# Kernel optimization log

Hardware: AMD Instinct MI355X
Metric: run time of the kernel (lower is better)

Reference implementation:

```python
import jax, jax.numpy as jnp
import numpy as np

B, N, F_IN = 8, 2048, 256
H, D = 4, 64  # num_heads, out_per_head (H*D == F_IN for residual)
ALPHA = 0.2   # leakyrelu slope


def setup_inputs() -> dict:
    key = jax.random.key(0)
    k1, k2, k3 = jax.random.split(key, 3)
    h = jax.random.normal(k1, (B, N, F_IN), dtype=jnp.float32)
    adj = jax.random.uniform(k2, (B, N, N), dtype=jnp.float32)
    # stacked per-head Linear weights (no bias): [H, F_in, D]
    W = jax.random.normal(k3, (H, F_IN, D), dtype=jnp.float32) * (1.0 / np.sqrt(F_IN))
    return {"h": h, "adj": adj, "W": W}


def reference(h, adj, W):
    # NOTE: in the original module, adj goes through drop_edge but is never
    # used in the attention computation, so it has no effect on the output.
    # P: per-head projections [B, H, N, D]
    P = jnp.einsum("bnf,hfd->bhnd", h, W)
    # scores: leakyrelu(P P^T) [B, H, N, N]
    scores = jnp.einsum("bhnd,bhmd->bhnm", P, P)
    scores = jnp.where(scores > 0, scores, ALPHA * scores)
    attn = jax.nn.softmax(scores, axis=-1)
    out = jnp.einsum("bhnm,bhmd->bhnd", attn, P)
    # concat heads along feature dim: [B, N, H*D]
    out = out.transpose(0, 2, 1, 3).reshape(h.shape[0], h.shape[1], -1)
    return out + h
```

## Files before the change

kernel.cpp:

```cpp
#include <hip/hip_runtime.h>
#include <cstdint>

#define B_    8
#define N_    2048
#define FIN_  256
#define H_    4
#define D_    64
#define NEG_SLOPE 0.2f
#define LOG2E 1.44269504f

typedef __bf16    bf16x8 __attribute__((ext_vector_type(8)));
typedef _Float16  f16x8  __attribute__((ext_vector_type(8)));
typedef __fp16    fp16x2 __attribute__((ext_vector_type(2)));
typedef uint16_t  u16x8  __attribute__((ext_vector_type(8)));
typedef float     fx4    __attribute__((ext_vector_type(4)));

static __device__ __forceinline__ float bf2f(uint16_t u) {
    union { uint32_t u; float f; } c; c.u = ((uint32_t)u) << 16; return c.f;
}
static __device__ __forceinline__ uint16_t f2bf(float f) {
    union { float f; uint32_t u; } c; c.f = f;
    return (uint16_t)((c.u + 0x7fffu + ((c.u >> 16) & 1u)) >> 16);
}
static __device__ __forceinline__ uint16_t f2h(float f) {
    const _Float16 h = (_Float16)f;
    return __builtin_bit_cast(uint16_t, h);
}
static __device__ __forceinline__ bf16x8 ldbf8(const uint16_t* p) {
    return *(const bf16x8*)p;
}
static __device__ __forceinline__ f16x8 ldf8(const uint16_t* p) {
    return *(const f16x8*)p;
}
static __device__ __forceinline__ bf16x8 asbf(u16x8 v) {
    union { u16x8 u; bf16x8 b; } c; c.u = v; return c.b;
}
static __device__ __forceinline__ void split8(const float* p, bf16x8& hi, bf16x8& lo) {
    const float4 x0 = *(const float4*)p;
    const float4 x1 = *(const float4*)(p + 4);
    const float f[8] = {x0.x, x0.y, x0.z, x0.w, x1.x, x1.y, x1.z, x1.w};
    u16x8 h, l;
    #pragma unroll
    for (int j = 0; j < 8; ++j) {
        const uint16_t hb = f2bf(f[j]);
        h[j] = hb;
        l[j] = f2bf(f[j] - bf2f(hb));
    }
    hi = asbf(h); lo = asbf(l);
}
static __device__ __forceinline__ uint32_t pkh2(float a, float b) {
    const fp16x2 h = __builtin_amdgcn_cvt_pkrtz(a, b);
    return __builtin_bit_cast(uint32_t, h);
}

__global__ void prep_kernel(const float* __restrict__ W,
                            uint16_t* __restrict__ Wt_hi,
                            uint16_t* __restrict__ Wt_lo) {
    const int h  = blockIdx.x >> 4;
    const int d4 = blockIdx.x & 15;
    const int f  = threadIdx.x;
    const float4 w = *(const float4*)(W + (((size_t)h * FIN_ + f) * D_ + d4 * 4));
    const float vv[4] = {w.x, w.y, w.z, w.w};
    #pragma unroll
    for (int j = 0; j < 4; ++j) {
        const int d = d4 * 4 + j;
        const uint16_t hb = f2bf(vv[j]);
        Wt_hi[((size_t)h * D_ + d) * FIN_ + f] = hb;
        Wt_lo[((size_t)h * D_ + d) * FIN_ + f] = f2bf(vv[j] - bf2f(hb));
    }
}

__global__ __launch_bounds__(256, 2) void proj_kernel(
    const float*    __restrict__ hin,
    const uint16_t* __restrict__ Wt_hi,
    const uint16_t* __restrict__ Wt_lo,
    uint16_t* __restrict__ P_f16,
    uint16_t* __restrict__ Pt_f16)
{
    __shared__ __align__(16) uint16_t plds[4][16][72];

    const int lane = threadIdx.x & 63, wave = threadIdx.x >> 6;
    const int quad = lane >> 4, l15 = lane & 15;

    const int b  = blockIdx.y;
    const int h0 = blockIdx.z * 2;
    const int n0 = blockIdx.x * 64 + wave * 16;

    const float* arow = hin + ((size_t)b * N_ + n0 + l15) * FIN_ + quad * 8;

    fx4 acc[2][4];
    #pragma unroll
    for (int hh = 0; hh < 2; ++hh)
        #pragma unroll
        for (int t = 0; t < 4; ++t) acc[hh][t] = (fx4)(0.0f);

    #pragma unroll
    for (int k0 = 0; k0 < FIN_; k0 += 32) {
        bf16x8 ahi, alo;
        split8(arow + k0, ahi, alo);
        #pragma unroll
        for (int hh = 0; hh < 2; ++hh) {
            const uint16_t* whi = Wt_hi + (size_t)(h0 + hh) * D_ * FIN_;
            const uint16_t* wlo = Wt_lo + (size_t)(h0 + hh) * D_ * FIN_;
            #pragma unroll
            for (int t = 0; t < 4; ++t) {
                const size_t off = (size_t)(t * 16 + l15) * FIN_ + k0 + quad * 8;
                const bf16x8 bhi = ldbf8(whi + off);
                const bf16x8 blo = ldbf8(wlo + off);
                acc[hh][t] = __builtin_amdgcn_mfma_f32_16x16x32_bf16(ahi, bhi, acc[hh][t], 0, 0, 0);
                acc[hh][t] = __builtin_amdgcn_mfma_f32_16x16x32_bf16(alo, bhi, acc[hh][t], 0, 0, 0);
                acc[hh][t] = __builtin_amdgcn_mfma_f32_16x16x32_bf16(ahi, blo, acc[hh][t], 0, 0, 0);
            }
        }
    }

    #pragma unroll
    for (int hh = 0; hh < 2; ++hh) {
        const int bh = b * H_ + h0 + hh;
        #pragma unroll
        for (int t = 0; t < 4; ++t)
            #pragma unroll
            for (int r = 0; r < 4; ++r)
                plds[wave][quad * 4 + r][t * 16 + l15] = f2h(acc[hh][t][r]);

        {
            const uint16_t* base = &plds[wave][l15][0];
            const int4 r0 = *(const int4*)(base + quad * 8);
            const int4 r1 = *(const int4*)(base + quad * 8 + 32);
            uint16_t* pg = P_f16 + ((size_t)bh * N_ + n0 + l15) * D_;
            *(int4*)(pg + quad * 8)      = r0;
            *(int4*)(pg + quad * 8 + 32) = r1;
        }
        {
            uint32_t u[8];
            #pragma unroll
            for (int j = 0; j < 8; ++j) {
                const uint16_t e0 = plds[wave][2 * j][lane];
                const uint16_t e1 = plds[wave][2 * j + 1][lane];
                u[j] = (uint32_t)e0 | ((uint32_t)e1 << 16);
            }
            uint16_t* pt = Pt_f16 + ((size_t)bh * D_ + lane) * N_ + n0;
            int4 s0, s1;
            s0.x = u[0]; s0.y = u[1]; s0.z = u[2]; s0.w = u[3];
            s1.x = u[4]; s1.y = u[5]; s1.z = u[6]; s1.w = u[7];
            *(int4*)pt       = s0;
            *(int4*)(pt + 8) = s1;
        }
    }
}

__global__ __launch_bounds__(256, 4) void attn_kernel(
    const uint16_t* __restrict__ P_f16,
    const uint16_t* __restrict__ Pt_f16,
    const float*    __restrict__ hin,
    float*          __restrict__ out)
{
    __shared__ __align__(16) uint16_t sK[64 * 64];
    __shared__ __align__(16) uint16_t sV[64 * 64];
    __shared__ __align__(16) uint16_t plds[4][16][72];

    const int tid  = threadIdx.x;
    const int lane = tid & 63, wave = tid >> 6;
    const int quad = lane >> 4, l15 = lane & 15;

    const int bh = blockIdx.y, b = bh >> 2, hd = bh & 3;
    const int n0 = blockIdx.x * 64 + wave * 16;

    const uint16_t* Pf = P_f16  + (size_t)bh * N_ * D_;
    const uint16_t* Pt = Pt_f16 + (size_t)bh * D_ * N_;

    f16x8 qf[2];
    {
        const uint16_t* qrow = Pf + (size_t)(n0 + l15) * D_ + quad * 8;
        qf[0] = ldf8(qrow); qf[1] = ldf8(qrow + 32);
        const _Float16 c = (_Float16)LOG2E;
        #pragma unroll
        for (int j = 0; j < 8; ++j) { qf[0][j] *= c; qf[1][j] *= c; }
    }

    const int i0 = tid, i1 = tid + 256;
    const int r0s = i0 >> 3, c0s = i0 & 7;
    const int r1s = i1 >> 3, c1s = i1 & 7;
    const uint16_t* gK0 = Pf + (size_t)r0s * D_ + (c0s ^ (r0s & 7)) * 8;
    const uint16_t* gK1 = Pf + (size_t)r1s * D_ + (c1s ^ (r1s & 7)) * 8;
    const uint16_t* gV0 = Pt + (size_t)r0s * N_ + (c0s ^ (r0s & 7)) * 8;
    const uint16_t* gV1 = Pt + (size_t)r1s * N_ + (c1s ^ (r1s & 7)) * 8;

    int4 rK0 = *(const int4*)gK0, rK1 = *(const int4*)gK1;
    int4 rV0 = *(const int4*)gV0, rV1 = *(const int4*)gV1;

    float m_i = -1e30f, l_i = 0.0f;
    fx4 oacc[4];
    #pragma unroll
    for (int dt = 0; dt < 4; ++dt) oacc[dt] = (fx4)(0.0f);

    const int cc = quad ^ (l15 & 7);

    for (int it = 0; it < N_ / 64; ++it) {
        __syncthreads();
        ((int4*)sK)[i0] = rK0; ((int4*)sK)[i1] = rK1;
        ((int4*)sV)[i0] = rV0; ((int4*)sV)[i1] = rV1;
        const int knx = (it < N_ / 64 - 1) ? (it + 1) * 64 : 0;
        rK0 = *(const int4*)(gK0 + (size_t)knx * D_);
        rK1 = *(const int4*)(gK1 + (size_t)knx * D_);
        rV0 = *(const int4*)(gV0 + knx);
        rV1 = *(const int4*)(gV1 + knx);
        __syncthreads();

        fx4 s[4];
        #pragma unroll
        for (int t = 0; t < 4; ++t) s[t] = (fx4)(0.0f);
        #pragma unroll
        for (int t = 0; t < 4; ++t) {
            const uint16_t* kb = sK + (t * 16 + l15) * 64;
            const f16x8 k0 = ldf8(kb + cc * 8);
            const f16x8 k1 = ldf8(kb + (cc ^ 4) * 8);
            s[t] = __builtin_amdgcn_mfma_f32_16x16x32_f16(k0, qf[0], s[t], 0, 0, 0);
            s[t] = __builtin_amdgcn_mfma_f32_16x16x32_f16(k1, qf[1], s[t], 0, 0, 0);
        }

        float pm[16];
        #pragma unroll
        for (int t = 0; t < 4; ++t)
            #pragma unroll
            for (int r = 0; r < 4; ++r) {
                const float v = s[t][r];
                pm[t * 4 + r] = fmaxf(v, NEG_SLOPE * v);
            }
        float mx = pm[0];
        #pragma unroll
        for (int j = 1; j < 16; ++j) mx = fmaxf(mx, pm[j]);
        mx = fmaxf(mx, __shfl_xor(mx, 16));
        mx = fmaxf(mx, __shfl_xor(mx, 32));
        const float mnew  = fmaxf(m_i, mx);
        const float alpha = __builtin_amdgcn_exp2f(m_i - mnew);
        float rs = 0.0f;
        #pragma unroll
        for (int j = 0; j < 16; ++j) {
            const float e = __builtin_amdgcn_exp2f(pm[j] - mnew);
            pm[j] = e; rs += e;
        }
        rs += __shfl_xor(rs, 16);
        rs += __shfl_xor(rs, 32);
        l_i = l_i * alpha + rs;
        m_i = mnew;
        #pragma unroll
        for (int dt = 0; dt < 4; ++dt)
            #pragma unroll
            for (int r = 0; r < 4; ++r) oacc[dt][r] *= alpha;

        #pragma unroll
        for (int t = 0; t < 4; ++t) {
            const uint32_t w0 = pkh2(pm[t * 4 + 0], pm[t * 4 + 1]);
            const uint32_t w1 = pkh2(pm[t * 4 + 2], pm[t * 4 + 3]);
            uint2* dst = (uint2*)&plds[wave][l15][t * 16 + quad * 4];
            *dst = make_uint2(w0, w1);
        }
        const f16x8 a0 = ldf8(&plds[wave][l15][quad * 8]);
        const f16x8 a1 = ldf8(&plds[wave][l15][32 + quad * 8]);

        #pragma unroll
        for (int dt = 0; dt < 4; ++dt) {
            const uint16_t* vb = sV + (dt * 16 + l15) * 64;
            const f16x8 v0 = ldf8(vb + cc * 8);
            const f16x8 v1 = ldf8(vb + (cc ^ 4) * 8);
            oacc[dt] = __builtin_amdgcn_mfma_f32_16x16x32_f16(v0, a0, oacc[dt], 0, 0, 0);
            oacc[dt] = __builtin_amdgcn_mfma_f32_16x16x32_f16(v1, a1, oacc[dt], 0, 0, 0);
        }
    }

    const float inv = 1.0f / l_i;
    const size_t rowbase = ((size_t)b * N_ + n0 + l15) * FIN_ + hd * D_;
    #pragma unroll
    for (int dt = 0; dt < 4; ++dt)
        #pragma unroll
        for (int r = 0; r < 4; ++r) {
            const size_t idx = rowbase + dt * 16 + quad * 4 + r;
            out[idx] = oacc[dt][r] * inv + hin[idx];
        }
}

extern "C" void kernel_launch(void* const* d_in, const int* in_sizes, int n_in,
                              void* d_out, int out_size, void* d_ws, size_t ws_size,
                              hipStream_t stream) {
    const float* hin = (const float*)d_in[0];
    const float* W   = (const float*)d_in[2];
    float* out = (float*)d_out;

    uint16_t* Wt_hi = (uint16_t*)d_ws;
    uint16_t* Wt_lo = Wt_hi + (size_t)H_ * D_ * FIN_;
    uint16_t* P_f16 = Wt_lo + (size_t)H_ * D_ * FIN_;
    uint16_t* Pt_f16= P_f16 + (size_t)B_ * H_ * N_ * D_;

    hipLaunchKernelGGL(prep_kernel, dim3(H_ * 16),         dim3(FIN_), 0, stream, W, Wt_hi, Wt_lo);
    hipLaunchKernelGGL(proj_kernel, dim3(N_/64, B_, H_/2), dim3(256),  0, stream,
                       hin, Wt_hi, Wt_lo, P_f16, Pt_f16);
    hipLaunchKernelGGL(attn_kernel, dim3(N_/64, B_*H_),    dim3(256),  0, stream,
                       P_f16, Pt_f16, hin, out);
}
```

Baseline: 278.3 us.

## Drop online softmax max, use self-score offset, bf16 PV, double-buffered 32-row tiles

The projection now uses a single fp16 MFMA per tile instead of a three-pass bf16 hi/lo split. The attention kernel removes the running-max online softmax and subtracts a fixed per-row offset instead: the query's own squared norm, which is the self-score. Row sums are computed with an MFMA against a ones vector, and P and V are stored as bf16, with P truncated rather than rounded. Each wave now handles 32 query rows, and K/V tiles are double-buffered in LDS with one barrier per iteration. In exchange, precision drops, and the fixed offset risks overflow or underflow if some score is far above the self-score.

Measured after the change: 253.0 us. 9.1% less time.

```diff
diff --git a/kernel.cpp b/kernel.cpp
--- a/kernel.cpp
+++ b/kernel.cpp
@@ -11,7 +11,6 @@
 
 typedef __bf16    bf16x8 __attribute__((ext_vector_type(8)));
 typedef _Float16  f16x8  __attribute__((ext_vector_type(8)));
-typedef __fp16    fp16x2 __attribute__((ext_vector_type(2)));
 typedef uint16_t  u16x8  __attribute__((ext_vector_type(8)));
 typedef float     fx4    __attribute__((ext_vector_type(4)));
 
@@ -32,30 +31,23 @@
 static __device__ __forceinline__ f16x8 ldf8(const uint16_t* p) {
     return *(const f16x8*)p;
 }
-static __device__ __forceinline__ bf16x8 asbf(u16x8 v) {
-    union { u16x8 u; bf16x8 b; } c; c.u = v; return c.b;
-}
-static __device__ __forceinline__ void split8(const float* p, bf16x8& hi, bf16x8& lo) {
+static __device__ __forceinline__ uint32_t pkbf_trunc(float lo, float hi) {
+    const uint32_t ul = __builtin_bit_cast(uint32_t, lo);
+    const uint32_t uh = __builtin_bit_cast(uint32_t, hi);
+    return (ul >> 16) | (uh & 0xFFFF0000u);
+}
+static __device__ __forceinline__ f16x8 cvt8(const float* p) {
     const float4 x0 = *(const float4*)p;
     const float4 x1 = *(const float4*)(p + 4);
     const float f[8] = {x0.x, x0.y, x0.z, x0.w, x1.x, x1.y, x1.z, x1.w};
-    u16x8 h, l;
-    #pragma unroll
-    for (int j = 0; j < 8; ++j) {
-        const uint16_t hb = f2bf(f[j]);
-        h[j] = hb;
-        l[j] = f2bf(f[j] - bf2f(hb));
-    }
-    hi = asbf(h); lo = asbf(l);
-}
-static __device__ __forceinline__ uint32_t pkh2(float a, float b) {
-    const fp16x2 h = __builtin_amdgcn_cvt_pkrtz(a, b);
-    return __builtin_bit_cast(uint32_t, h);
+    f16x8 r;
+    #pragma unroll
+    for (int j = 0; j < 8; ++j) r[j] = (_Float16)f[j];
+    return r;
 }
 
 __global__ void prep_kernel(const float* __restrict__ W,
-                            uint16_t* __restrict__ Wt_hi,
-                            uint16_t* __restrict__ Wt_lo) {
+                            uint16_t* __restrict__ Wt_f16) {
     const int h  = blockIdx.x >> 4;
     const int d4 = blockIdx.x & 15;
     const int f  = threadIdx.x;
@@ -64,18 +56,15 @@
     #pragma unroll
     for (int j = 0; j < 4; ++j) {
         const int d = d4 * 4 + j;
-        const uint16_t hb = f2bf(vv[j]);
-        Wt_hi[((size_t)h * D_ + d) * FIN_ + f] = hb;
-        Wt_lo[((size_t)h * D_ + d) * FIN_ + f] = f2bf(vv[j] - bf2f(hb));
+        Wt_f16[((size_t)h * D_ + d) * FIN_ + f] = f2h(vv[j]);
     }
 }
 
 __global__ __launch_bounds__(256, 2) void proj_kernel(
     const float*    __restrict__ hin,
-    const uint16_t* __restrict__ Wt_hi,
-    const uint16_t* __restrict__ Wt_lo,
+    const uint16_t* __restrict__ Wt_f16,
     uint16_t* __restrict__ P_f16,
-    uint16_t* __restrict__ Pt_f16)
+    uint16_t* __restrict__ Pt_bf16)
 {
     __shared__ __align__(16) uint16_t plds[4][16][72];
 
@@ -96,20 +85,14 @@
 
     #pragma unroll
     for (int k0 = 0; k0 < FIN_; k0 += 32) {
-        bf16x8 ahi, alo;
-        split8(arow + k0, ahi, alo);
+        const f16x8 a = cvt8(arow + k0);
         #pragma unroll
         for (int hh = 0; hh < 2; ++hh) {
-            const uint16_t* whi = Wt_hi + (size_t)(h0 + hh) * D_ * FIN_;
-            const uint16_t* wlo = Wt_lo + (size_t)(h0 + hh) * D_ * FIN_;
+            const uint16_t* wb = Wt_f16 + (size_t)(h0 + hh) * D_ * FIN_;
             #pragma unroll
             for (int t = 0; t < 4; ++t) {
-                const size_t off = (size_t)(t * 16 + l15) * FIN_ + k0 + quad * 8;
-                const bf16x8 bhi = ldbf8(whi + off);
-                const bf16x8 blo = ldbf8(wlo + off);
-                acc[hh][t] = __builtin_amdgcn_mfma_f32_16x16x32_bf16(ahi, bhi, acc[hh][t], 0, 0, 0);
-                acc[hh][t] = __builtin_amdgcn_mfma_f32_16x16x32_bf16(alo, bhi, acc[hh][t], 0, 0, 0);
-                acc[hh][t] = __builtin_amdgcn_mfma_f32_16x16x32_bf16(ahi, blo, acc[hh][t], 0, 0, 0);
+                const f16x8 bb = ldf8(wb + (size_t)(t * 16 + l15) * FIN_ + k0 + quad * 8);
+                acc[hh][t] = __builtin_amdgcn_mfma_f32_16x16x32_f16(a, bb, acc[hh][t], 0, 0, 0);
             }
         }
     }
@@ -122,7 +105,6 @@
             #pragma unroll
             for (int r = 0; r < 4; ++r)
                 plds[wave][quad * 4 + r][t * 16 + l15] = f2h(acc[hh][t][r]);
-
         {
             const uint16_t* base = &plds[wave][l15][0];
             const int4 r0 = *(const int4*)(base + quad * 8);
@@ -131,6 +113,11 @@
             *(int4*)(pg + quad * 8)      = r0;
             *(int4*)(pg + quad * 8 + 32) = r1;
         }
+        #pragma unroll
+        for (int t = 0; t < 4; ++t)
+            #pragma unroll
+            for (int r = 0; r < 4; ++r)
+                plds[wave][quad * 4 + r][t * 16 + l15] = f2bf(acc[hh][t][r]);
         {
             uint32_t u[8];
             #pragma unroll
@@ -139,7 +126,7 @@
                 const uint16_t e1 = plds[wave][2 * j + 1][lane];
                 u[j] = (uint32_t)e0 | ((uint32_t)e1 << 16);
             }
-            uint16_t* pt = Pt_f16 + ((size_t)bh * D_ + lane) * N_ + n0;
+            uint16_t* pt = Pt_bf16 + ((size_t)bh * D_ + lane) * N_ + n0;
             int4 s0, s1;
             s0.x = u[0]; s0.y = u[1]; s0.z = u[2]; s0.w = u[3];
             s1.x = u[4]; s1.y = u[5]; s1.z = u[6]; s1.w = u[7];
@@ -149,33 +136,56 @@
     }
 }
 
-__global__ __launch_bounds__(256, 4) void attn_kernel(
+__global__ __launch_bounds__(256, 2) void attn_kernel(
     const uint16_t* __restrict__ P_f16,
-    const uint16_t* __restrict__ Pt_f16,
+    const uint16_t* __restrict__ Pt_bf16,
     const float*    __restrict__ hin,
     float*          __restrict__ out)
 {
-    __shared__ __align__(16) uint16_t sK[64 * 64];
-    __shared__ __align__(16) uint16_t sV[64 * 64];
-    __shared__ __align__(16) uint16_t plds[4][16][72];
+    __shared__ __align__(16) uint16_t sK[2][64 * 64];
+    __shared__ __align__(16) uint16_t sV[2][64 * 64];
+    __shared__ __align__(16) uint16_t plds[4][32][72];
 
     const int tid  = threadIdx.x;
     const int lane = tid & 63, wave = tid >> 6;
     const int quad = lane >> 4, l15 = lane & 15;
 
     const int bh = blockIdx.y, b = bh >> 2, hd = bh & 3;
-    const int n0 = blockIdx.x * 64 + wave * 16;
-
-    const uint16_t* Pf = P_f16  + (size_t)bh * N_ * D_;
-    const uint16_t* Pt = Pt_f16 + (size_t)bh * D_ * N_;
-
-    f16x8 qf[2];
+    const int n0 = blockIdx.x * 128 + wave * 32;
+
+    const uint16_t* Pf = P_f16   + (size_t)bh * N_ * D_;
+    const uint16_t* Pt = Pt_bf16 + (size_t)bh * D_ * N_;
+
+    f16x8 qf[2][2];
+    #pragma unroll
+    for (int mt = 0; mt < 2; ++mt) {
+        const uint16_t* qrow = Pf + (size_t)(n0 + mt * 16 + l15) * D_ + quad * 8;
+        qf[mt][0] = ldf8(qrow); qf[mt][1] = ldf8(qrow + 32);
+        const _Float16 c = (_Float16)LOG2E;
+        #pragma unroll
+        for (int j = 0; j < 8; ++j) { qf[mt][0][j] *= c; qf[mt][1][j] *= c; }
+    }
+
+    float C[2];
+    #pragma unroll
+    for (int mt = 0; mt < 2; ++mt) {
+        float acc = 0.0f;
+        #pragma unroll
+        for (int j = 0; j < 8; ++j) {
+            const float a0 = (float)qf[mt][0][j], a1 = (float)qf[mt][1][j];
+            acc += a0 * a0 + a1 * a1;
+        }
+        acc += __shfl_xor(acc, 16);
+        acc += __shfl_xor(acc, 32);
+        C[mt] = acc * (1.0f / LOG2E);
+    }
+
+    bf16x8 ones;
     {
-        const uint16_t* qrow = Pf + (size_t)(n0 + l15) * D_ + quad * 8;
-        qf[0] = ldf8(qrow); qf[1] = ldf8(qrow + 32);
-        const _Float16 c = (_Float16)LOG2E;
-        #pragma unroll
-        for (int j = 0; j < 8; ++j) { qf[0][j] *= c; qf[1][j] *= c; }
+        u16x8 ov;
+        #pragma unroll
+        for (int j = 0; j < 8; ++j) ov[j] = 0x3F80;
+        ones = __builtin_bit_cast(bf16x8, ov);
     }
 
     const int i0 = tid, i1 = tid + 256;
@@ -186,98 +196,118 @@
     const uint16_t* gV0 = Pt + (size_t)r0s * N_ + (c0s ^ (r0s & 7)) * 8;
     const uint16_t* gV1 = Pt + (size_t)r1s * N_ + (c1s ^ (r1s & 7)) * 8;
 
-    int4 rK0 = *(const int4*)gK0, rK1 = *(const int4*)gK1;
-    int4 rV0 = *(const int4*)gV0, rV1 = *(const int4*)gV1;
-
-    float m_i = -1e30f, l_i = 0.0f;
-    fx4 oacc[4];
-    #pragma unroll
-    for (int dt = 0; dt < 4; ++dt) oacc[dt] = (fx4)(0.0f);
+    {
+        int4 a = *(const int4*)gK0, bb = *(const int4*)gK1;
+        int4 c = *(const int4*)gV0, d  = *(const int4*)gV1;
+        ((int4*)sK[0])[i0] = a;  ((int4*)sK[0])[i1] = bb;
+        ((int4*)sV[0])[i0] = c;  ((int4*)sV[0])[i1] = d;
+    }
+    int4 rK0 = *(const int4*)(gK0 + (size_t)64 * D_);
+    int4 rK1 = *(const int4*)(gK1 + (size_t)64 * D_);
+    int4 rV0 = *(const int4*)(gV0 + 64);
+    int4 rV1 = *(const int4*)(gV1 + 64);
+
+    fx4 oacc[2][4], lacc[2];
+    #pragma unroll
+    for (int mt = 0; mt < 2; ++mt) {
+        lacc[mt] = (fx4)(0.0f);
+        #pragma unroll
+        for (int dt = 0; dt < 4; ++dt) oacc[mt][dt] = (fx4)(0.0f);
+    }
 
     const int cc = quad ^ (l15 & 7);
 
+    __syncthreads();
     for (int it = 0; it < N_ / 64; ++it) {
-        __syncthreads();
-        ((int4*)sK)[i0] = rK0; ((int4*)sK)[i1] = rK1;
-        ((int4*)sV)[i0] = rV0; ((int4*)sV)[i1] = rV1;
-        const int knx = (it < N_ / 64 - 1) ? (it + 1) * 64 : 0;
-        rK0 = *(const int4*)(gK0 + (size_t)knx * D_);
-        rK1 = *(const int4*)(gK1 + (size_t)knx * D_);
-        rV0 = *(const int4*)(gV0 + knx);
-        rV1 = *(const int4*)(gV1 + knx);
-        __syncthreads();
-
-        fx4 s[4];
-        #pragma unroll
-        for (int t = 0; t < 4; ++t) s[t] = (fx4)(0.0f);
+        const int cur = it & 1;
+        if (it < N_ / 64 - 1) {
+            ((int4*)sK[cur ^ 1])[i0] = rK0; ((int4*)sK[cur ^ 1])[i1] = rK1;
+            ((int4*)sV[cur ^ 1])[i0] = rV0; ((int4*)sV[cur ^ 1])[i1] = rV1;
+        }
+        if (it < N_ / 64 - 2) {
+            const size_t ko = (size_t)(it + 2) * 64;
+            rK0 = *(const int4*)(gK0 + ko * D_);
+            rK1 = *(const int4*)(gK1 + ko * D_);
+            rV0 = *(const int4*)(gV0 + ko);
+            rV1 = *(const int4*)(gV1 + ko);
+        }
+
+        fx4 s[2][4];
+        #pragma unroll
+        for (int mt = 0; mt < 2; ++mt)
+            #pragma unroll
+            for (int t = 0; t < 4; ++t) s[mt][t] = (fx4)(0.0f);
         #pragma unroll
         for (int t = 0; t < 4; ++t) {
-            const uint16_t* kb = sK + (t * 16 + l15) * 64;
+            const uint16_t* kb = &sK[cur][(t * 16 + l15) * 64];
             const f16x8 k0 = ldf8(kb + cc * 8);
             const f16x8 k1 = ldf8(kb + (cc ^ 4) * 8);
-            s[t] = __builtin_amdgcn_mfma_f32_16x16x32_f16(k0, qf[0], s[t], 0, 0, 0);
-            s[t] = __builtin_amdgcn_mfma_f32_16x16x32_f16(k1, qf[1], s[t], 0, 0, 0);
-        }
-
-        float pm[16];
-        #pragma unroll
-        for (int t = 0; t < 4; ++t)
-            #pragma unroll
-            for (int r = 0; r < 4; ++r) {
-                const float v = s[t][r];
-                pm[t * 4 + r] = fmaxf(v, NEG_SLOPE * v);
-            }
-        float mx = pm[0];
-        #pragma unroll
-        for (int j = 1; j < 16; ++j) mx = fmaxf(mx, pm[j]);
-        mx = fmaxf(mx, __shfl_xor(mx, 16));
-        mx = fmaxf(mx, __shfl_xor(mx, 32));
-        const float mnew  = fmaxf(m_i, mx);
-        const float alpha = __builtin_amdgcn_exp2f(m_i - mnew);
-        float rs = 0.0f;
-        #pragma unroll
-        for (int j = 0; j < 16; ++j) {
-            const float e = __builtin_amdgcn_exp2f(pm[j] - mnew);
-            pm[j] = e; rs += e;
-        }
-        rs += __shfl_xor(rs, 16);
-        rs += __shfl_xor(rs, 32);
-        l_i = l_i * alpha + rs;
-        m_i = mnew;
-        #pragma unroll
-        for (int dt = 0; dt < 4; ++dt)
-            #pragma unroll
-            for (int r = 0; r < 4; ++r) oacc[dt][r] *= alpha;
-
-        #pragma unroll
-        for (int t = 0; t < 4; ++t) {
-            const uint32_t w0 = pkh2(pm[t * 4 + 0], pm[t * 4 + 1]);
-            const uint32_t w1 = pkh2(pm[t * 4 + 2], pm[t * 4 + 3]);
-            uint2* dst = (uint2*)&plds[wave][l15][t * 16 + quad * 4];
-            *dst = make_uint2(w0, w1);
-        }
-        const f16x8 a0 = ldf8(&plds[wave][l15][quad * 8]);
-        const f16x8 a1 = ldf8(&plds[wave][l15][32 + quad * 8]);
-
+            #pragma unroll
+            for (int mt = 0; mt < 2; ++mt) {
+                s[mt][t] = __builtin_amdgcn_mfma_f32_16x16x32_f16(k0, qf[mt][0], s[mt][t], 0, 0, 0);
+                s[mt][t] = __builtin_amdgcn_mfma_f32_16x16x32_f16(k1, qf[mt][1], s[mt][t], 0, 0, 0);
+            }
+        }
+
+        #pragma unroll
+        for (int mt = 0; mt < 2; ++mt) {
+            #pragma unroll
+            for (int t = 0; t < 4; ++t) {
+                float e[4];
+                #pragma unroll
+                for (int r = 0; r < 4; ++r) {
+                    const float v = s[mt][t][r];
+                    e[r] = __builtin_amdgcn_exp2f(fmaxf(v, NEG_SLOPE * v) - C[mt]);
+                }
+                const uint32_t w0 = pkbf_trunc(e[0], e[1]);
+                const uint32_t w1 = pkbf_trunc(e[2], e[3]);
+                *(uint2*)&plds[wave][mt * 16 + l15][t * 16 + quad * 4] = make_uint2(w0, w1);
+            }
+        }
+
+        bf16x8 a[2][2];
+        #pragma unroll
+        for (int mt = 0; mt < 2; ++mt) {
+            const uint16_t* pb = &plds[wave][mt * 16 + l15][0];
+            a[mt][0] = ldbf8(pb + quad * 8);
+            a[mt][1] = ldbf8(pb + quad * 8 + 32);
+        }
+
+        #pragma unroll
+        for (int mt = 0; mt < 2; ++mt) {
+            lacc[mt] = __builtin_amdgcn_mfma_f32_16x16x32_bf16(ones, a[mt][0], lacc[mt], 0, 0, 0);
+            lacc[mt] = __builtin_amdgcn_mfma_f32_16x16x32_bf16(ones, a[mt][1], lacc[mt], 0, 0, 0);
+        }
         #pragma unroll
         for (int dt = 0; dt < 4; ++dt) {
-            const uint16_t* vb = sV + (dt * 16 + l15) * 64;
-            const f16x8 v0 = ldf8(vb + cc * 8);
-            const f16x8 v1 = ldf8(vb + (cc ^ 4) * 8);
-            oacc[dt] = __builtin_amdgcn_mfma_f32_16x16x32_f16(v0, a0, oacc[dt], 0, 0, 0);
-            oacc[dt] = __builtin_amdgcn_mfma_f32_16x16x32_f16(v1, a1, oacc[dt], 0, 0, 0);
-        }
-    }
-
-    const float inv = 1.0f / l_i;
-    const size_t rowbase = ((size_t)b * N_ + n0 + l15) * FIN_ + hd * D_;
-    #pragma unroll
-    for (int dt = 0; dt < 4; ++dt)
-        #pragma unroll
-        for (int r = 0; r < 4; ++r) {
-            const size_t idx = rowbase + dt * 16 + quad * 4 + r;
-            out[idx] = oacc[dt][r] * inv + hin[idx];
-        }
+            const uint16_t* vb = &sV[cur][(dt * 16 + l15) * 64];
+            const bf16x8 v0 = ldbf8(vb + cc * 8);
+            const bf16x8 v1 = ldbf8(vb + (cc ^ 4) * 8);
+            #pragma unroll
+            for (int mt = 0; mt < 2; ++mt) {
+                oacc[mt][dt] = __builtin_amdgcn_mfma_f32_16x16x32_bf16(v0, a[mt][0], oacc[mt][dt], 0, 0, 0);
+                oacc[mt][dt] = __builtin_amdgcn_mfma_f32_16x16x32_bf16(v1, a[mt][1], oacc[mt][dt], 0, 0, 0);
+            }
+        }
+        __syncthreads();
+    }
+
+    #pragma unroll
+    for (int mt = 0; mt < 2; ++mt) {
+        const float inv = 1.0f / lacc[mt][0];
+        const size_t rowbase = ((size_t)b * N_ + n0 + mt * 16 + l15) * FIN_ + hd * D_;
+        #pragma unroll
+        for (int dt = 0; dt < 4; ++dt) {
+            const size_t idx = rowbase + dt * 16 + quad * 4;
+            const float4 hv = *(const float4*)&hin[idx];
+            float4 o;
+            o.x = oacc[mt][dt][0] * inv + hv.x;
+            o.y = oacc[mt][dt][1] * inv + hv.y;
+            o.z = oacc[mt][dt][2] * inv + hv.z;
+            o.w = oacc[mt][dt][3] * inv + hv.w;
+            *(float4*)&out[idx] = o;
+        }
+    }
 }
 
 extern "C" void kernel_launch(void* const* d_in, const int* in_sizes, int n_in,
@@ -287,14 +317,13 @@
     const float* W   = (const float*)d_in[2];
     float* out = (float*)d_out;
 
-    uint16_t* Wt_hi = (uint16_t*)d_ws;
-    uint16_t* Wt_lo = Wt_hi + (size_t)H_ * D_ * FIN_;
-    uint16_t* P_f16 = Wt_lo + (size_t)H_ * D_ * FIN_;
-    uint16_t* Pt_f16= P_f16 + (size_t)B_ * H_ * N_ * D_;
-
-    hipLaunchKernelGGL(prep_kernel, dim3(H_ * 16),         dim3(FIN_), 0, stream, W, Wt_hi, Wt_lo);
+    uint16_t* Wt_f16  = (uint16_t*)d_ws;
+    uint16_t* P_f16   = Wt_f16 + (size_t)H_ * D_ * FIN_;
+    uint16_t* Pt_bf16 = P_f16  + (size_t)B_ * H_ * N_ * D_;
+
+    hipLaunchKernelGGL(prep_kernel, dim3(H_ * 16),         dim3(FIN_), 0, stream, W, Wt_f16);
     hipLaunchKernelGGL(proj_kernel, dim3(N_/64, B_, H_/2), dim3(256),  0, stream,
-                       hin, Wt_hi, Wt_lo, P_f16, Pt_f16);
-    hipLaunchKernelGGL(attn_kernel, dim3(N_/64, B_*H_),    dim3(256),  0, stream,
-                       P_f16, Pt_f16, hin, out);
-}
+                       hin, Wt_f16, P_f16, Pt_bf16);
+    hipLaunchKernelGGL(attn_kernel, dim3(N_/128, B_*H_),   dim3(256),  0, stream,
+                       P_f16, Pt_bf16, hin, out);
+}
```
